# Kernel optimization log

Measured on AMD Instinct MI355X. Metric: run time of the kernel, lower is better.

## Reference

```python
import jax, jax.numpy as jnp
import numpy as np

B, T, D_MODEL, H, DH = 4, 2048, 768, 12, 64


def _rope_tables(T, dh):
    # standard rotary frequencies, (T, dh//2)
    inv_freq = 1.0 / (10000.0 ** (np.arange(0, dh, 2, dtype=np.float32) / dh))
    t = np.arange(T, dtype=np.float32)
    ang = np.outer(t, inv_freq)  # (T, dh//2)
    return jnp.asarray(np.cos(ang)), jnp.asarray(np.sin(ang))


def setup_inputs() -> dict:
    key = jax.random.key(0)
    ks = jax.random.split(key, 5)
    scale = 1.0 / np.sqrt(D_MODEL)
    x = jax.random.normal(ks[0], (B, T, D_MODEL), dtype=jnp.float32)
    wq = jax.random.normal(ks[1], (D_MODEL, D_MODEL), dtype=jnp.float32) * scale
    wk = jax.random.normal(ks[2], (D_MODEL, D_MODEL), dtype=jnp.float32) * scale
    wv = jax.random.normal(ks[3], (D_MODEL, D_MODEL), dtype=jnp.float32) * scale
    wo = jax.random.normal(ks[4], (D_MODEL, D_MODEL), dtype=jnp.float32) * scale
    rope_cos, rope_sin = _rope_tables(T, DH)
    return {"x": x, "rope_cos": rope_cos, "rope_sin": rope_sin,
            "wq": wq, "wk": wk, "wv": wv, "wo": wo}


def _apply_rope(x, cos, sin):
    # x: (B, H, T, DH), cos/sin: (T, DH//2) -> interleaved rotation
    t = x.shape[2]
    c = cos[:t][None, None]  # (1,1,T,DH//2)
    s = sin[:t][None, None]
    x1 = x[..., ::2]
    x2 = x[..., 1::2]
    return jnp.stack([x1 * c - x2 * s, x1 * s + x2 * c], axis=-1).reshape(x.shape)


def reference(x, rope_cos, rope_sin, wq, wk, wv, wo):
    b, t, _ = x.shape
    # Linear (torch nn.Linear: y = x @ W.T), split heads -> (B,H,T,DH)
    q = (x @ wq.T).reshape(b, t, H, DH).transpose(0, 2, 1, 3)
    k = (x @ wk.T).reshape(b, t, H, DH).transpose(0, 2, 1, 3)
    v = (x @ wv.T).reshape(b, t, H, DH).transpose(0, 2, 1, 3)
    q = _apply_rope(q, rope_cos, rope_sin)
    k = _apply_rope(k, rope_cos, rope_sin)
    scores = jnp.einsum("bhqd,bhkd->bhqk", q, k) * (DH ** -0.5)
    causal = jnp.tril(jnp.ones((t, t), dtype=bool))  # (T,T)
    scores = jnp.where(causal[None, None], scores, -jnp.inf)
    attn = jax.nn.softmax(scores, axis=-1)
    out = jnp.einsum("bhqk,bhkd->bhqd", attn, v)
    out = out.transpose(0, 2, 1, 3).reshape(b, t, H * DH)
    return out @ wo.T
```

## Files before the change

kernel.cpp:

```cpp
#include <hip/hip_runtime.h>
#include <hip/hip_bf16.h>
#include <math.h>

#define B_ 4
#define T_ 2048
#define DM 768
#define H_ 12
#define DH 64

typedef __attribute__((ext_vector_type(4))) float f32x4;
typedef __attribute__((ext_vector_type(8))) short s16x8;

typedef const __attribute__((address_space(1))) void* gas1_t;
typedef __attribute__((address_space(3))) void* las3_t;

__device__ __forceinline__ ushort f2b(float f) {
  union { float f; unsigned u; } v; v.f = f;
  unsigned u = v.u;
  u += 0x7fffu + ((u >> 16) & 1u);
  return (ushort)(u >> 16);
}
__device__ __forceinline__ unsigned cvt_pk_bf16(float lo, float hi) {
  unsigned r;
  asm("v_cvt_pk_bf16_f32 %0, %1, %2" : "=v"(r) : "v"(lo), "v"(hi));
  return r;
}

__global__ void cvt_all(const float* __restrict__ x,
                        const float* __restrict__ wq, const float* __restrict__ wk,
                        const float* __restrict__ wv, const float* __restrict__ wo,
                        const float* __restrict__ rc, const float* __restrict__ rs,
                        ushort* __restrict__ xb, ushort* __restrict__ wqkv,
                        ushort* __restrict__ wob, float2* __restrict__ cs2) {
  const int bid = blockIdx.x, t = threadIdx.x;
  if (bid < 6144) {
    int i = bid * 256 + t;
    float4 v = ((const float4*)x)[i];
    ushort4 o;
    o.x = f2b(v.x); o.y = f2b(v.y); o.z = f2b(v.z); o.w = f2b(v.w);
    ((ushort4*)xb)[i] = o;
  } else if (bid < 8448) {
    int i = (bid - 6144) * 256 + t;
    int which = i / 147456, j = i - which * 147456;
    const float* src = which == 0 ? wq : which == 1 ? wk : which == 2 ? wv : wo;
    ushort* dst = which < 3 ? wqkv + (size_t)which * 589824 : wob;
    float4 v = ((const float4*)src)[j];
    ushort4 o;
    o.x = f2b(v.x); o.y = f2b(v.y); o.z = f2b(v.z); o.w = f2b(v.w);
    ((ushort4*)dst)[j] = o;
  } else {
    int i = (bid - 8448) * 256 + t;
    cs2[i] = make_float2(rc[i], rs[i]);
  }
}

__global__ __launch_bounds__(256, 3) void gemm_qkv(
    const ushort* __restrict__ A, const ushort* __restrict__ Bw,
    const float2* __restrict__ cs2,
    ushort* __restrict__ Qb, ushort* __restrict__ Kb, ushort* __restrict__ Vt) {
  const int K = 768;
  __shared__ ushort As[128 * 64];
  __shared__ ushort Bs[192 * 64];
  const int bid = blockIdx.x;
  const int xcd = bid & 7;
  const int jj = bid >> 3;
  const int mloc = jj / 12, nn0 = jj - mloc * 12;
  const int m0 = (xcd * 8 + mloc) * 128, n0 = nn0 * 192;
  const int tid = threadIdx.x;
  const int wave = tid >> 6, lane = tid & 63;
  const int wm = (wave >> 1) * 64, wn = (wave & 1) * 96;
  const int quad = lane >> 4, l16 = lane & 15;
  const int tr = tid >> 3;
  const int scb = (tid & 7) ^ (tr & 7);
  const int swz = l16 & 7;

  f32x4 acc[4][6] = {};

  const ushort* ga = A + (size_t)(m0 + tr) * K + scb * 8;
  const ushort* gb = Bw + (size_t)(n0 + tr) * K + scb * 8;

  for (int k0 = 0; k0 < K; k0 += 64) {
#pragma unroll
    for (int p = 0; p < 4; p++)
      __builtin_amdgcn_global_load_lds((gas1_t)(ga + (size_t)(p * 32) * K + k0),
                                       (las3_t)(As + p * 2048 + tid * 8), 16, 0, 0);
#pragma unroll
    for (int p = 0; p < 6; p++)
      __builtin_amdgcn_global_load_lds((gas1_t)(gb + (size_t)(p * 32) * K + k0),
                                       (las3_t)(Bs + p * 2048 + tid * 8), 16, 0, 0);
    __syncthreads();
#pragma unroll
    for (int kk = 0; kk < 2; kk++) {
      s16x8 af[4], bf[6];
#pragma unroll
      for (int i = 0; i < 4; i++) {
        const ushort* ar = As + (wm + i * 16 + l16) * 64;
        af[i] = *(const s16x8*)(ar + (((kk * 4 + quad) ^ swz) * 8));
      }
#pragma unroll
      for (int n = 0; n < 6; n++) {
        const ushort* br = Bs + (wn + n * 16 + l16) * 64;
        bf[n] = *(const s16x8*)(br + (((kk * 4 + quad) ^ swz) * 8));
      }
#pragma unroll
      for (int i = 0; i < 4; i++)
#pragma unroll
        for (int n = 0; n < 6; n++)
          acc[i][n] = __builtin_amdgcn_mfma_f32_16x16x32_bf16(af[i], bf[n], acc[i][n], 0, 0, 0);
    }
    __syncthreads();
  }

  const int sec = n0 / 768;
  if (sec < 2) {
    ushort* dst = sec == 0 ? Qb : Kb;
#pragma unroll
    for (int i = 0; i < 4; i++) {
      int row0 = m0 + wm + i * 16 + quad * 4;
#pragma unroll
      for (int nt = 0; nt < 6; nt++) {
        int col = n0 + wn + nt * 16 + l16;
        int nv = col - sec * 768;
        int h = nv >> 6, d = nv & 63;
        int ip = (d >> 1) & 31;
        float sgn = (d & 1) ? 1.f : -1.f;
#pragma unroll
        for (int r = 0; r < 4; r++) {
          int rrow = row0 + r;
          int t = rrow & (T_ - 1), bb = rrow >> 11;
          float v = acc[i][nt][r];
          float partner = __shfl_xor(v, 1);
          float2 cs = cs2[t * 32 + ip];
          float out = fmaf(v, cs.x, sgn * partner * cs.y);
          dst[((size_t)(bb * H_ + h) * T_ + t) * DH + d] = f2b(out);
        }
      }
    }
  } else {
#pragma unroll
    for (int i = 0; i < 4; i++) {
      int row0 = m0 + wm + i * 16 + quad * 4;
      int t0 = row0 & (T_ - 1), b = row0 >> 11;
#pragma unroll
      for (int nt = 0; nt < 6; nt++) {
        int col = n0 + wn + nt * 16 + l16;
        int nv = col - 1536;
        int h = nv >> 6, d = nv & 63;
        ushort4 pk;
        pk.x = f2b(acc[i][nt][0]); pk.y = f2b(acc[i][nt][1]);
        pk.z = f2b(acc[i][nt][2]); pk.w = f2b(acc[i][nt][3]);
        *(ushort4*)(Vt + ((size_t)(b * H_ + h) * DH + d) * T_ + t0) = pk;
      }
    }
  }
}

__global__ __launch_bounds__(256, 3) void gemm_out(
    const ushort* __restrict__ A, const ushort* __restrict__ Bw, float* __restrict__ C) {
  const int K = 768, N = 768;
  __shared__ ushort As[128 * 64];
  __shared__ ushort Bs[96 * 64];
  const int bid = blockIdx.x;
  const int xcd = bid & 7;
  const int jj = bid >> 3;
  const int mloc = jj >> 3, nn0 = jj & 7;
  const int m0 = (xcd * 8 + mloc) * 128, n0 = nn0 * 96;
  const int tid = threadIdx.x;
  const int wave = tid >> 6, lane = tid & 63;
  const int wm = (wave >> 1) * 64, wn = (wave & 1) * 48;
  const int quad = lane >> 4, l16 = lane & 15;
  const int tr = tid >> 3;
  const int scb = (tid & 7) ^ (tr & 7);
  const int swz = l16 & 7;

  f32x4 acc[4][3] = {};

  const ushort* ga = A + (size_t)(m0 + tr) * K + scb * 8;
  const ushort* gb = Bw + (size_t)(n0 + tr) * K + scb * 8;

  for (int k0 = 0; k0 < K; k0 += 64) {
#pragma unroll
    for (int p = 0; p < 4; p++)
      __builtin_amdgcn_global_load_lds((gas1_t)(ga + (size_t)(p * 32) * K + k0),
                                       (las3_t)(As + p * 2048 + tid * 8), 16, 0, 0);
#pragma unroll
    for (int p = 0; p < 3; p++)
      __builtin_amdgcn_global_load_lds((gas1_t)(gb + (size_t)(p * 32) * K + k0),
                                       (las3_t)(Bs + p * 2048 + tid * 8), 16, 0, 0);
    __syncthreads();
#pragma unroll
    for (int kk = 0; kk < 2; kk++) {
      s16x8 af[4], bf[3];
#pragma unroll
      for (int i = 0; i < 4; i++) {
        const ushort* ar = As + (wm + i * 16 + l16) * 64;
        af[i] = *(const s16x8*)(ar + (((kk * 4 + quad) ^ swz) * 8));
      }
#pragma unroll
      for (int n = 0; n < 3; n++) {
        const ushort* br = Bs + (wn + n * 16 + l16) * 64;
        bf[n] = *(const s16x8*)(br + (((kk * 4 + quad) ^ swz) * 8));
      }
#pragma unroll
      for (int i = 0; i < 4; i++)
#pragma unroll
        for (int n = 0; n < 3; n++)
          acc[i][n] = __builtin_amdgcn_mfma_f32_16x16x32_bf16(af[i], bf[n], acc[i][n], 0, 0, 0);
    }
    __syncthreads();
  }

#pragma unroll
  for (int i = 0; i < 4; i++) {
    int row = m0 + wm + i * 16 + quad * 4;
#pragma unroll
    for (int n = 0; n < 3; n++) {
      int col = n0 + wn + n * 16 + l16;
#pragma unroll
      for (int r = 0; r < 4; r++)
        C[(size_t)(row + r) * N + col] = acc[i][n][r];
    }
  }
}

#define EXP2SCALE 0.18033688f
#define EXP2OFF  17.312340f
__global__ __launch_bounds__(256, 3) void attn(const ushort* __restrict__ Qb, const ushort* __restrict__ Kb,
                                               const ushort* __restrict__ Vt, ushort* __restrict__ Ob) {
  const int bh = blockIdx.x;
  const int p = blockIdx.y;
  const int tid = threadIdx.x, wave = tid >> 6, lane = tid & 63;
  const int quad = lane >> 4, l16 = lane & 15;
  const int b = bh / H_, h = bh % H_;
  const ushort* Qp = Qb + (size_t)bh * T_ * DH;
  const ushort* Kp = Kb + (size_t)bh * T_ * DH;
  const ushort* Vp = Vt + (size_t)bh * DH * T_;

  __shared__ ushort Ks[2][64 * 64];
  __shared__ ushort Vs[2][64 * 64];
  __shared__ ushort P[4][16][72];

  const int myTile = (wave < 2) ? p : (31 - p);
  const int qbase0 = myTile * 64 + (wave & 1) * 32;

  s16x8 aq[2][2];
#pragma unroll
  for (int m = 0; m < 2; m++) {
    const ushort* qp = Qp + (size_t)(qbase0 + m * 16 + l16) * DH + quad * 8;
    aq[m][0] = *(const s16x8*)qp;
    aq[m][1] = *(const s16x8*)(qp + 32);
  }
  f32x4 o[2][4] = {};
  float rsum[2] = {0.f, 0.f};

  const int ntile = 32 - p;
  const int srow = tid >> 3;
  const int scbK = (tid & 7) ^ (srow & 7);
  const int swz = (l16 & 7);

  {
    const int kv0 = 0;
    __builtin_amdgcn_global_load_lds((gas1_t)(Kp + (size_t)(kv0 + srow) * DH + scbK * 8),
                                     (las3_t)(Ks[0] + tid * 8), 16, 0, 0);
    __builtin_amdgcn_global_load_lds((gas1_t)(Kp + (size_t)(kv0 + srow + 32) * DH + scbK * 8),
                                     (las3_t)(Ks[0] + 2048 + tid * 8), 16, 0, 0);
    __builtin_amdgcn_global_load_lds((gas1_t)(Vp + (size_t)srow * T_ + kv0 + scbK * 8),
                                     (las3_t)(Vs[0] + tid * 8), 16, 0, 0);
    __builtin_amdgcn_global_load_lds((gas1_t)(Vp + (size_t)(srow + 32) * T_ + kv0 + scbK * 8),
                                     (las3_t)(Vs[0] + 2048 + tid * 8), 16, 0, 0);
  }

  for (int c = 0; c < ntile; c++) {
    const int kv0 = c * 64;
    const int cur = c & 1;
    __syncthreads();
    if (c + 1 < ntile) {
      const int kv1 = kv0 + 64, nxt = cur ^ 1;
      __builtin_amdgcn_global_load_lds((gas1_t)(Kp + (size_t)(kv1 + srow) * DH + scbK * 8),
                                       (las3_t)(Ks[nxt] + tid * 8), 16, 0, 0);
      __builtin_amdgcn_global_load_lds((gas1_t)(Kp + (size_t)(kv1 + srow + 32) * DH + scbK * 8),
                                       (las3_t)(Ks[nxt] + 2048 + tid * 8), 16, 0, 0);
      __builtin_amdgcn_global_load_lds((gas1_t)(Vp + (size_t)srow * T_ + kv1 + scbK * 8),
                                       (las3_t)(Vs[nxt] + tid * 8), 16, 0, 0);
      __builtin_amdgcn_global_load_lds((gas1_t)(Vp + (size_t)(srow + 32) * T_ + kv1 + scbK * 8),
                                       (las3_t)(Vs[nxt] + 2048 + tid * 8), 16, 0, 0);
    }

    if (kv0 <= qbase0 + 31) {
      s16x8 kf[4][2];
#pragma unroll
      for (int nt = 0; nt < 4; nt++) {
        const ushort* kr = Ks[cur] + (nt * 16 + l16) * 64;
        kf[nt][0] = *(const s16x8*)(kr + ((quad ^ swz) * 8));
        kf[nt][1] = *(const s16x8*)(kr + (((4 + quad) ^ swz) * 8));
      }
      s16x8 bv[4][2];
#pragma unroll
      for (int dt = 0; dt < 4; dt++) {
        const ushort* vr = Vs[cur] + (dt * 16 + l16) * 64;
        bv[dt][0] = *(const s16x8*)(vr + ((quad ^ swz) * 8));
        bv[dt][1] = *(const s16x8*)(vr + (((4 + quad) ^ swz) * 8));
      }

#pragma unroll
      for (int m = 0; m < 2; m++) {
        const int qb = qbase0 + m * 16;
        if (kv0 > qb + 15) continue;
        f32x4 s[4] = {};
#pragma unroll
        for (int nt = 0; nt < 4; nt++) {
          s[nt] = __builtin_amdgcn_mfma_f32_16x16x32_bf16(kf[nt][0], aq[m][0], s[nt], 0, 0, 0);
          s[nt] = __builtin_amdgcn_mfma_f32_16x16x32_bf16(kf[nt][1], aq[m][1], s[nt], 0, 0, 0);
        }
        if (kv0 + 63 <= qb) {
#pragma unroll
          for (int nt = 0; nt < 4; nt++) {
            float p0 = __builtin_amdgcn_exp2f(fmaf(s[nt][0], EXP2SCALE, -EXP2OFF));
            float p1 = __builtin_amdgcn_exp2f(fmaf(s[nt][1], EXP2SCALE, -EXP2OFF));
            float p2 = __builtin_amdgcn_exp2f(fmaf(s[nt][2], EXP2SCALE, -EXP2OFF));
            float p3 = __builtin_amdgcn_exp2f(fmaf(s[nt][3], EXP2SCALE, -EXP2OFF));
            rsum[m] += (p0 + p1) + (p2 + p3);
            uint2 pk;
            pk.x = cvt_pk_bf16(p0, p1);
            pk.y = cvt_pk_bf16(p2, p3);
            *(uint2*)&P[wave][l16][nt * 16 + quad * 4] = pk;
          }
        } else {
          int qi = qb + l16;
#pragma unroll
          for (int nt = 0; nt < 4; nt++) {
            int kvb = kv0 + nt * 16 + quad * 4;
            float pv[4];
#pragma unroll
            for (int r = 0; r < 4; r++)
              pv[r] = (kvb + r <= qi) ? __builtin_amdgcn_exp2f(fmaf(s[nt][r], EXP2SCALE, -EXP2OFF)) : 0.f;
            rsum[m] += (pv[0] + pv[1]) + (pv[2] + pv[3]);
            uint2 pk;
            pk.x = cvt_pk_bf16(pv[0], pv[1]);
            pk.y = cvt_pk_bf16(pv[2], pv[3]);
            *(uint2*)&P[wave][l16][nt * 16 + quad * 4] = pk;
          }
        }
        s16x8 ap0 = *(const s16x8*)&P[wave][l16][quad * 8];
        s16x8 ap1 = *(const s16x8*)&P[wave][l16][32 + quad * 8];
#pragma unroll
        for (int dt = 0; dt < 4; dt++) {
          o[m][dt] = __builtin_amdgcn_mfma_f32_16x16x32_bf16(ap0, bv[dt][0], o[m][dt], 0, 0, 0);
          o[m][dt] = __builtin_amdgcn_mfma_f32_16x16x32_bf16(ap1, bv[dt][1], o[m][dt], 0, 0, 0);
        }
      }
    }
  }
#pragma unroll
  for (int m = 0; m < 2; m++) {
    rsum[m] += __shfl_xor(rsum[m], 16);
    rsum[m] += __shfl_xor(rsum[m], 32);
  }
#pragma unroll
  for (int m = 0; m < 2; m++)
#pragma unroll
    for (int r = 0; r < 4; r++) {
      float inv = 1.0f / __shfl(rsum[m], quad * 4 + r);
      int q = qbase0 + m * 16 + quad * 4 + r;
#pragma unroll
      for (int dt = 0; dt < 4; dt++)
        Ob[(size_t)(b * T_ + q) * DM + h * 64 + dt * 16 + l16] = f2b(o[m][dt][r] * inv);
    }
}

extern "C" void kernel_launch(void* const* d_in, const int* in_sizes, int n_in,
                              void* d_out, int out_size, void* d_ws, size_t ws_size,
                              hipStream_t stream) {
  const float* x = (const float*)d_in[0];
  const float* rc = (const float*)d_in[1];
  const float* rs = (const float*)d_in[2];
  const float* wq = (const float*)d_in[3];
  const float* wk = (const float*)d_in[4];
  const float* wv = (const float*)d_in[5];
  const float* wo = (const float*)d_in[6];

  char* ws = (char*)d_ws;
  ushort* xb   = (ushort*)(ws);
  ushort* wqkv = (ushort*)(ws + 12582912);
  ushort* wob  = (ushort*)(ws + 16121856);
  float2* cs2  = (float2*)(ws + 17301504);
  ushort* Qb   = (ushort*)(ws + 17825792);
  ushort* Kb   = (ushort*)(ws + 30408704);
  ushort* Vt   = (ushort*)(ws + 42991616);
  ushort* Ob   = (ushort*)(ws + 55574528);

  cvt_all<<<8704, 256, 0, stream>>>(x, wq, wk, wv, wo, rc, rs, xb, wqkv, wob, cs2);

  gemm_qkv<<<768, 256, 0, stream>>>(xb, wqkv, cs2, Qb, Kb, Vt);

  attn<<<dim3(48, 16), 256, 0, stream>>>(Qb, Kb, Vt, Ob);

  gemm_out<<<512, 256, 0, stream>>>(Ob, wob, (float*)d_out);
}
```

Baseline: 188.0 us.

## Halve per-wave query rows in attention and double grid, swizzle P buffer

Each wave now handles 16 query rows instead of 32. Blocks pair 32-row tiles (p and 63-p), and the grid doubles to 1536 blocks to give more parallelism and better balance of causal work across CUs. The P scratch buffer drops its padding and uses an XOR swizzle to avoid LDS bank conflicts. In exchange, each K/V tile loaded into LDS is reused by fewer query rows, which raises total K/V global traffic.

```diff
diff --git a/kernel.cpp b/kernel.cpp
--- a/kernel.cpp
+++ b/kernel.cpp
@@ -238,25 +238,25 @@
 
   __shared__ ushort Ks[2][64 * 64];
   __shared__ ushort Vs[2][64 * 64];
-  __shared__ ushort P[4][16][72];
-
-  const int myTile = (wave < 2) ? p : (31 - p);
-  const int qbase0 = myTile * 64 + (wave & 1) * 32;
-
-  s16x8 aq[2][2];
-#pragma unroll
-  for (int m = 0; m < 2; m++) {
-    const ushort* qp = Qp + (size_t)(qbase0 + m * 16 + l16) * DH + quad * 8;
-    aq[m][0] = *(const s16x8*)qp;
-    aq[m][1] = *(const s16x8*)(qp + 32);
-  }
-  f32x4 o[2][4] = {};
-  float rsum[2] = {0.f, 0.f};
-
-  const int ntile = 32 - p;
+  __shared__ ushort P[4][16][64];
+
+  const int myTile = (wave < 2) ? p : (63 - p);
+  const int qb = myTile * 32 + (wave & 1) * 16;
+
+  s16x8 aq[2];
+  {
+    const ushort* qp = Qp + (size_t)(qb + l16) * DH + quad * 8;
+    aq[0] = *(const s16x8*)qp;
+    aq[1] = *(const s16x8*)(qp + 32);
+  }
+  f32x4 o[4] = {};
+  float rsum = 0.f;
+
+  const int ntile = ((2047 - 32 * p) >> 6) + 1;
   const int srow = tid >> 3;
   const int scbK = (tid & 7) ^ (srow & 7);
   const int swz = (l16 & 7);
+  const int psw = swz << 3;
 
   {
     const int kv0 = 0;
@@ -286,7 +286,7 @@
                                        (las3_t)(Vs[nxt] + 2048 + tid * 8), 16, 0, 0);
     }
 
-    if (kv0 <= qbase0 + 31) {
+    if (kv0 <= qb + 15) {
       s16x8 kf[4][2];
 #pragma unroll
       for (int nt = 0; nt < 4; nt++) {
@@ -302,70 +302,62 @@
         bv[dt][1] = *(const s16x8*)(vr + (((4 + quad) ^ swz) * 8));
       }
 
-#pragma unroll
-      for (int m = 0; m < 2; m++) {
-        const int qb = qbase0 + m * 16;
-        if (kv0 > qb + 15) continue;
-        f32x4 s[4] = {};
+      f32x4 s[4] = {};
+#pragma unroll
+      for (int nt = 0; nt < 4; nt++) {
+        s[nt] = __builtin_amdgcn_mfma_f32_16x16x32_bf16(kf[nt][0], aq[0], s[nt], 0, 0, 0);
+        s[nt] = __builtin_amdgcn_mfma_f32_16x16x32_bf16(kf[nt][1], aq[1], s[nt], 0, 0, 0);
+      }
+      if (kv0 + 63 <= qb) {
 #pragma unroll
         for (int nt = 0; nt < 4; nt++) {
-          s[nt] = __builtin_amdgcn_mfma_f32_16x16x32_bf16(kf[nt][0], aq[m][0], s[nt], 0, 0, 0);
-          s[nt] = __builtin_amdgcn_mfma_f32_16x16x32_bf16(kf[nt][1], aq[m][1], s[nt], 0, 0, 0);
+          float p0 = __builtin_amdgcn_exp2f(fmaf(s[nt][0], EXP2SCALE, -EXP2OFF));
+          float p1 = __builtin_amdgcn_exp2f(fmaf(s[nt][1], EXP2SCALE, -EXP2OFF));
+          float p2 = __builtin_amdgcn_exp2f(fmaf(s[nt][2], EXP2SCALE, -EXP2OFF));
+          float p3 = __builtin_amdgcn_exp2f(fmaf(s[nt][3], EXP2SCALE, -EXP2OFF));
+          rsum += (p0 + p1) + (p2 + p3);
+          int sc = (nt * 16 + quad * 4) ^ psw;
+          uint2 pk;
+          pk.x = cvt_pk_bf16(p0, p1);
+          pk.y = cvt_pk_bf16(p2, p3);
+          *(uint2*)&P[wave][l16][sc] = pk;
         }
-        if (kv0 + 63 <= qb) {
-#pragma unroll
-          for (int nt = 0; nt < 4; nt++) {
-            float p0 = __builtin_amdgcn_exp2f(fmaf(s[nt][0], EXP2SCALE, -EXP2OFF));
-            float p1 = __builtin_amdgcn_exp2f(fmaf(s[nt][1], EXP2SCALE, -EXP2OFF));
-            float p2 = __builtin_amdgcn_exp2f(fmaf(s[nt][2], EXP2SCALE, -EXP2OFF));
-            float p3 = __builtin_amdgcn_exp2f(fmaf(s[nt][3], EXP2SCALE, -EXP2OFF));
-            rsum[m] += (p0 + p1) + (p2 + p3);
-            uint2 pk;
-            pk.x = cvt_pk_bf16(p0, p1);
-            pk.y = cvt_pk_bf16(p2, p3);
-            *(uint2*)&P[wave][l16][nt * 16 + quad * 4] = pk;
-          }
-        } else {
-          int qi = qb + l16;
-#pragma unroll
-          for (int nt = 0; nt < 4; nt++) {
-            int kvb = kv0 + nt * 16 + quad * 4;
-            float pv[4];
-#pragma unroll
-            for (int r = 0; r < 4; r++)
-              pv[r] = (kvb + r <= qi) ? __builtin_amdgcn_exp2f(fmaf(s[nt][r], EXP2SCALE, -EXP2OFF)) : 0.f;
-            rsum[m] += (pv[0] + pv[1]) + (pv[2] + pv[3]);
-            uint2 pk;
-            pk.x = cvt_pk_bf16(pv[0], pv[1]);
-            pk.y = cvt_pk_bf16(pv[2], pv[3]);
-            *(uint2*)&P[wave][l16][nt * 16 + quad * 4] = pk;
-          }
+      } else {
+        int qi = qb + l16;
+#pragma unroll
+        for (int nt = 0; nt < 4; nt++) {
+          int kvb = kv0 + nt * 16 + quad * 4;
+          float pv[4];
+#pragma unroll
+          for (int r = 0; r < 4; r++)
+            pv[r] = (kvb + r <= qi) ? __builtin_amdgcn_exp2f(fmaf(s[nt][r], EXP2SCALE, -EXP2OFF)) : 0.f;
+          rsum += (pv[0] + pv[1]) + (pv[2] + pv[3]);
+          int sc = (nt * 16 + quad * 4) ^ psw;
+          uint2 pk;
+          pk.x = cvt_pk_bf16(pv[0], pv[1]);
+          pk.y = cvt_pk_bf16(pv[2], pv[3]);
+          *(uint2*)&P[wave][l16][sc] = pk;
         }
-        s16x8 ap0 = *(const s16x8*)&P[wave][l16][quad * 8];
-        s16x8 ap1 = *(const s16x8*)&P[wave][l16][32 + quad * 8];
-#pragma unroll
-        for (int dt = 0; dt < 4; dt++) {
-          o[m][dt] = __builtin_amdgcn_mfma_f32_16x16x32_bf16(ap0, bv[dt][0], o[m][dt], 0, 0, 0);
-          o[m][dt] = __builtin_amdgcn_mfma_f32_16x16x32_bf16(ap1, bv[dt][1], o[m][dt], 0, 0, 0);
-        }
-      }
-    }
-  }
-#pragma unroll
-  for (int m = 0; m < 2; m++) {
-    rsum[m] += __shfl_xor(rsum[m], 16);
-    rsum[m] += __shfl_xor(rsum[m], 32);
-  }
-#pragma unroll
-  for (int m = 0; m < 2; m++)
-#pragma unroll
-    for (int r = 0; r < 4; r++) {
-      float inv = 1.0f / __shfl(rsum[m], quad * 4 + r);
-      int q = qbase0 + m * 16 + quad * 4 + r;
-#pragma unroll
-      for (int dt = 0; dt < 4; dt++)
-        Ob[(size_t)(b * T_ + q) * DM + h * 64 + dt * 16 + l16] = f2b(o[m][dt][r] * inv);
-    }
+      }
+      s16x8 ap0 = *(const s16x8*)&P[wave][l16][(quad * 8) ^ psw];
+      s16x8 ap1 = *(const s16x8*)&P[wave][l16][(32 + quad * 8) ^ psw];
+#pragma unroll
+      for (int dt = 0; dt < 4; dt++) {
+        o[dt] = __builtin_amdgcn_mfma_f32_16x16x32_bf16(ap0, bv[dt][0], o[dt], 0, 0, 0);
+        o[dt] = __builtin_amdgcn_mfma_f32_16x16x32_bf16(ap1, bv[dt][1], o[dt], 0, 0, 0);
+      }
+    }
+  }
+  rsum += __shfl_xor(rsum, 16);
+  rsum += __shfl_xor(rsum, 32);
+#pragma unroll
+  for (int r = 0; r < 4; r++) {
+    float inv = 1.0f / __shfl(rsum, quad * 4 + r);
+    int q = qb + quad * 4 + r;
+#pragma unroll
+    for (int dt = 0; dt < 4; dt++)
+      Ob[(size_t)(b * T_ + q) * DM + h * 64 + dt * 16 + l16] = f2b(o[dt][r] * inv);
+  }
 }
 
 extern "C" void kernel_launch(void* const* d_in, const int* in_sizes, int n_in,
@@ -393,7 +385,7 @@
 
   gemm_qkv<<<768, 256, 0, stream>>>(xb, wqkv, cs2, Qb, Kb, Vt);
 
-  attn<<<dim3(48, 16), 256, 0, stream>>>(Qb, Kb, Vt, Ob);
+  attn<<<dim3(48, 32), 256, 0, stream>>>(Qb, Kb, Vt, Ob);
 
   gemm_out<<<512, 256, 0, stream>>>(Ob, wob, (float*)d_out);
 }
```

Result: slower. 205.7 us (+9.4%).
